# Kernel optimization log

Measured on AMD Instinct MI355X. Metric: run time of the kernel, lower is better.

The kernel has to match this reference:

```python
import jax, jax.numpy as jnp
import numpy as np

N = 1024          # number of junctions
H = 1024          # heatmap height
W = 1024          # heatmap width
NUM_SAMPLES = 64  # samples along each candidate segment (torch_sampler)
DETECT_THRESH = 0.5
INLIER_THRESH = 0.99


def setup_inputs() -> dict:
    key = jax.random.key(0)
    k1, k2 = jax.random.split(key)
    # junctions are (h, w) float coordinates inside the image
    junctions = jax.random.uniform(k1, (N, 2), dtype=jnp.float32) * (H - 1)
    heatmap = jax.random.uniform(k2, (H, W), dtype=jnp.float32)
    return {"junctions": junctions, "heatmap": heatmap}


def _bilinear_sample(heatmap, ch, cw):
    """SOLD2 detect_bilinear: gather 4 corners, bilinear weights. ch/cw: [N,N,S]."""
    hf = jnp.floor(ch); hc = jnp.ceil(ch)
    wf = jnp.floor(cw); wc = jnp.ceil(cw)
    hfi = hf.astype(jnp.int32); hci = hc.astype(jnp.int32)
    wfi = wf.astype(jnp.int32); wci = wc.astype(jnp.int32)
    return (heatmap[hfi, wfi] * (hc - ch) * (wc - cw)
          + heatmap[hfi, wci] * (hc - ch) * (cw - wf)
          + heatmap[hci, wfi] * (ch - hf) * (wc - cw)
          + heatmap[hci, wci] * (ch - hf) * (cw - wf))


def reference(junctions, heatmap):
    n = junctions.shape[0]
    Hh, Ww = heatmap.shape
    t = jnp.linspace(0.0, 1.0, NUM_SAMPLES, dtype=jnp.float32)  # [S]
    # cand_samples[i, j, s] = junc[i] * t[s] + junc[j] * (1 - t[s])  (start=i, end=j)
    ch = junctions[:, None, 0:1] * t + junctions[None, :, 0:1] * (1.0 - t)  # [N,N,S]
    cw = junctions[:, None, 1:2] * t + junctions[None, :, 1:2] * (1.0 - t)  # [N,N,S]
    ch = jnp.clip(ch, 0.0, Hh - 1)
    cw = jnp.clip(cw, 0.0, Ww - 1)
    feat = _bilinear_sample(heatmap, ch, cw)                    # [N,N,S]
    mean_feat = feat.mean(axis=-1)                              # [N,N]
    inlier_ratio = (feat > DETECT_THRESH).astype(jnp.float32).mean(axis=-1)
    # candidate map: strict upper triangle (torch.triu(ones, diagonal=1))
    cand_mask = jnp.triu(jnp.ones((n, n), dtype=bool), k=1)
    detected = (mean_feat > DETECT_THRESH) & (inlier_ratio >= INLIER_THRESH) & cand_mask
    line_map = (detected | detected.T).astype(jnp.int32)        # symmetric line map
    return line_map, mean_feat
```

## Files before the change

kernel.cpp:

```cpp
#include <hip/hip_runtime.h>

#define NJ 1024
#define DETECT 0.5f
#define RESCUE 0.4975f

__device__ __forceinline__ float sample_t(int s) {
    return (s == 63) ? 1.0f : (float)s * (1.0f / 63.0f);
}

__device__ __forceinline__ void exact_pair(const float2 ja, const float2 jb,
                                           const float* __restrict__ heat,
                                           float& mean_o, float& min_o)
{
    float acc = 0.0f;
    float mn  = __builtin_inff();
    for (int s = 0; s < 64; ++s) {
        const float t  = sample_t(s);
        const float om = 1.0f - t;
        float ch = __fadd_rn(__fmul_rn(ja.x, t), __fmul_rn(jb.x, om));
        float cw = __fadd_rn(__fmul_rn(ja.y, t), __fmul_rn(jb.y, om));
        ch = fminf(fmaxf(ch, 0.0f), 1023.0f);
        cw = fminf(fmaxf(cw, 0.0f), 1023.0f);
        const float hf = floorf(ch), hc = ceilf(ch);
        const float wf = floorf(cw), wc = ceilf(cw);
        const int hfi = (int)hf, hci = (int)hc;
        const int wfi = (int)wf, wci = (int)wc;
        const float a00 = heat[(hfi << 10) + wfi];
        const float a01 = heat[(hfi << 10) + wci];
        const float a10 = heat[(hci << 10) + wfi];
        const float a11 = heat[(hci << 10) + wci];
        const float t1 = __fmul_rn(__fmul_rn(a00, __fsub_rn(hc, ch)), __fsub_rn(wc, cw));
        const float t2 = __fmul_rn(__fmul_rn(a01, __fsub_rn(hc, ch)), __fsub_rn(cw, wf));
        const float t3 = __fmul_rn(__fmul_rn(a10, __fsub_rn(ch, hf)), __fsub_rn(wc, cw));
        const float t4 = __fmul_rn(__fmul_rn(a11, __fsub_rn(ch, hf)), __fsub_rn(cw, wf));
        const float feat = __fadd_rn(__fadd_rn(__fadd_rn(t1, t2), t3), t4);
        acc += feat;
        mn = fminf(mn, feat);
    }
    mean_o = acc * (1.0f / 64.0f);
    min_o  = mn;
}

__global__ __launch_bounds__(256) void pack_kernel(
    const float* __restrict__ heat, uint4* __restrict__ packed4)
{
    const int idx = blockIdx.x * 256 + threadIdx.x;
    const int h = idx >> 8;
    const int w4 = (idx & 255) << 2;
    const int hn = (h < 1023) ? h + 1 : 1023;
    const float* r0 = heat + (h  << 10);
    const float* r1 = heat + (hn << 10);
    const float4 a = *(const float4*)(r0 + w4);
    const float4 b = *(const float4*)(r1 + w4);
    const int wnext = (w4 + 4 <= 1023) ? w4 + 4 : 1023;
    const float a4 = r0[wnext];
    const float b4 = r1[wnext];

    const float av[5] = {a.x, a.y, a.z, a.w, a4};
    const float bv[5] = {b.x, b.y, b.z, b.w, b4};
    unsigned int out[4];
    #pragma unroll
    for (int u = 0; u < 4; ++u) {
        const unsigned int c0 = (unsigned int)__float2int_rn(av[u]     * 255.0f);
        const unsigned int c1 = (unsigned int)__float2int_rn(av[u + 1] * 255.0f);
        const unsigned int c2 = (unsigned int)__float2int_rn(bv[u]     * 255.0f);
        const unsigned int c3 = (unsigned int)__float2int_rn(bv[u + 1] * 255.0f);
        out[u] = c0 | (c1 << 8) | (c2 << 16) | (c3 << 24);
    }
    packed4[idx] = make_uint4(out[0], out[1], out[2], out[3]);
}

__global__ __launch_bounds__(256) void sold2_thread_kernel(
    const float* __restrict__ junc,
    const float* __restrict__ heat,
    const unsigned int* __restrict__ packed,
    float* __restrict__ line_out,
    float* __restrict__ mean_out)
{
    const int q = blockIdx.x * 256 + threadIdx.x;
    const int r = q / 513;
    const int c = q - r * 513;
    const int j = (r + c) & 1023;

    const float2 jr  = ((const float2*)junc)[r];
    const float2 jjc = ((const float2*)junc)[j];

    float acc = 0.0f;
    float mn  = __builtin_inff();

    #pragma unroll
    for (int s0 = 0; s0 < 64; s0 += 16) {
        float chv[16], cwv[16];
        unsigned int cv[16];
        #pragma unroll
        for (int u = 0; u < 16; ++u) {
            const int s = s0 + u;
            const float t  = sample_t(s);
            const float om = 1.0f - t;
            float ch = __fadd_rn(__fmul_rn(jr.x, t), __fmul_rn(jjc.x, om));
            float cw = __fadd_rn(__fmul_rn(jr.y, t), __fmul_rn(jjc.y, om));
            ch = fminf(fmaxf(ch, 0.0f), 1023.0f);
            cw = fminf(fmaxf(cw, 0.0f), 1023.0f);
            chv[u] = ch;
            cwv[u] = cw;
            const int hfi = (int)ch;
            const int wfi = (int)cw;
            cv[u] = packed[(hfi << 10) + wfi];
        }
        #pragma unroll
        for (int u = 0; u < 16; ++u) {
            const float ch = chv[u], cw = cwv[u];
            const float hf = floorf(ch), hc = ceilf(ch);
            const float wf = floorf(cw), wc = ceilf(cw);
            const float wh0 = hc - ch, wh1 = ch - hf;
            const float ww0 = wc - cw, ww1 = cw - wf;
            const unsigned int cc = cv[u];
            const float a00 = (float)(cc & 0xffu);
            const float a01 = (float)((cc >> 8) & 0xffu);
            const float a10 = (float)((cc >> 16) & 0xffu);
            const float a11 = (float)(cc >> 24);
            const float feat = a00 * (wh0 * ww0) + a01 * (wh0 * ww1)
                             + a10 * (wh1 * ww0) + a11 * (wh1 * ww1);
            acc += feat;
            mn = fminf(mn, feat);
        }
    }

    float mean = acc * (1.0f / (255.0f * 64.0f));
    const float mns = mn * (1.0f / 255.0f);

    bool det = false;
    if ((mns > RESCUE) && (mean > RESCUE) && (c != 0)) {
        float mn2;
        exact_pair(jr, jjc, heat, mean, mn2);
        det = (mean > DETECT) && (mn2 > DETECT);
    }

    const int p1 = (r << 10) + j;
    __builtin_nontemporal_store(mean, mean_out + p1);
    __builtin_nontemporal_store(det ? 1.0f : 0.0f, line_out + p1);
}

__global__ __launch_bounds__(256) void mirror_kernel(
    float* __restrict__ line_out, float* __restrict__ mean_out)
{
    __shared__ float lm[64][65];
    __shared__ float mm[64][65];
    const int bi = blockIdx.x >> 4;
    const int bj = blockIdx.x & 15;

    const int D = ((bj - bi) << 6) & 1023;
    if (D >= 63 && D <= 449) return;

    const int tx = threadIdx.x & 63;
    const int g  = threadIdx.x >> 6;

    #pragma unroll
    for (int k = 0; k < 16; ++k) {
        const int b = (g << 4) + k;
        const int src = ((bj << 6) + b) * 1024 + (bi << 6) + tx;
        lm[b][tx] = line_out[src];
        mm[b][tx] = mean_out[src];
    }
    __syncthreads();

    #pragma unroll
    for (int k = 0; k < 16; ++k) {
        const int a = (g << 4) + k;
        const int i = (bi << 6) + a;
        const int j = (bj << 6) + tx;
        const int d = (j - i) & 1023;
        if (d >= 513) {
            const int dst = i * 1024 + j;
            __builtin_nontemporal_store(lm[tx][a], line_out + dst);
            __builtin_nontemporal_store(mm[tx][a], mean_out + dst);
        }
    }
}

extern "C" void kernel_launch(void* const* d_in, const int* in_sizes, int n_in,
                              void* d_out, int out_size, void* d_ws, size_t ws_size,
                              hipStream_t stream) {
    const float* junc = (const float*)d_in[0];
    const float* heat = (const float*)d_in[1];
    float* line_out = (float*)d_out;
    float* mean_out = line_out + NJ * NJ;

    unsigned int* packed = (unsigned int*)d_ws;
    pack_kernel<<<1024, 256, 0, stream>>>(heat, (uint4*)packed);

    const int total = NJ * 513;
    sold2_thread_kernel<<<total / 256, 256, 0, stream>>>(junc, heat, packed,
                                                         line_out, mean_out);

    mirror_kernel<<<256, 256, 0, stream>>>(line_out, mean_out);
}
```

Baseline: 186.9 us.

## Software-pipeline packed heatmap gathers with triple-buffered loads and sched barriers

Restructures the sampling loop so three batches of 16 gathers are in flight before any are consumed, rotating buffers so the fourth batch is issued while the first is processed. Sample coordinates are recomputed in the consume phase from opaque copies of the junction values instead of being kept in registers, and scheduling barriers pin the issue/consume order. Launch bounds now request six waves per SIMD to hold occupancy while 48 outstanding loads sit in registers. The aim is to hide gather latency; the cost is extra recomputed arithmetic and higher register pressure, which could cause spills.

```diff
diff --git a/kernel.cpp b/kernel.cpp
--- a/kernel.cpp
+++ b/kernel.cpp
@@ -70,7 +70,7 @@
     packed4[idx] = make_uint4(out[0], out[1], out[2], out[3]);
 }
 
-__global__ __launch_bounds__(256) void sold2_thread_kernel(
+__global__ __launch_bounds__(256, 6) void sold2_thread_kernel(
     const float* __restrict__ junc,
     const float* __restrict__ heat,
     const unsigned int* __restrict__ packed,
@@ -85,46 +85,65 @@
     const float2 jr  = ((const float2*)junc)[r];
     const float2 jjc = ((const float2*)junc)[j];
 
+    float jrx = jr.x, jry = jr.y, jjx = jjc.x, jjy = jjc.y;
+    asm volatile("" : "+v"(jrx), "+v"(jry), "+v"(jjx), "+v"(jjy));
+
     float acc = 0.0f;
     float mn  = __builtin_inff();
 
-    #pragma unroll
-    for (int s0 = 0; s0 < 64; s0 += 16) {
-        float chv[16], cwv[16];
-        unsigned int cv[16];
-        #pragma unroll
-        for (int u = 0; u < 16; ++u) {
-            const int s = s0 + u;
-            const float t  = sample_t(s);
-            const float om = 1.0f - t;
-            float ch = __fadd_rn(__fmul_rn(jr.x, t), __fmul_rn(jjc.x, om));
-            float cw = __fadd_rn(__fmul_rn(jr.y, t), __fmul_rn(jjc.y, om));
-            ch = fminf(fmaxf(ch, 0.0f), 1023.0f);
-            cw = fminf(fmaxf(cw, 0.0f), 1023.0f);
-            chv[u] = ch;
-            cwv[u] = cw;
-            const int hfi = (int)ch;
-            const int wfi = (int)cw;
-            cv[u] = packed[(hfi << 10) + wfi];
-        }
-        #pragma unroll
-        for (int u = 0; u < 16; ++u) {
-            const float ch = chv[u], cw = cwv[u];
-            const float hf = floorf(ch), hc = ceilf(ch);
-            const float wf = floorf(cw), wc = ceilf(cw);
-            const float wh0 = hc - ch, wh1 = ch - hf;
-            const float ww0 = wc - cw, ww1 = cw - wf;
-            const unsigned int cc = cv[u];
-            const float a00 = (float)(cc & 0xffu);
-            const float a01 = (float)((cc >> 8) & 0xffu);
-            const float a10 = (float)((cc >> 16) & 0xffu);
-            const float a11 = (float)(cc >> 24);
-            const float feat = a00 * (wh0 * ww0) + a01 * (wh0 * ww1)
-                             + a10 * (wh1 * ww0) + a11 * (wh1 * ww1);
-            acc += feat;
-            mn = fminf(mn, feat);
-        }
-    }
+    unsigned int cvA[16], cvB[16], cvC[16];
+
+#define ISSUE(S0, CV)                                                         \
+    _Pragma("unroll")                                                         \
+    for (int u = 0; u < 16; ++u) {                                            \
+        const int s = (S0) + u;                                               \
+        const float t  = sample_t(s);                                         \
+        const float om = 1.0f - t;                                            \
+        float ch = __fadd_rn(__fmul_rn(jr.x, t), __fmul_rn(jjc.x, om));       \
+        float cw = __fadd_rn(__fmul_rn(jr.y, t), __fmul_rn(jjc.y, om));       \
+        ch = fminf(fmaxf(ch, 0.0f), 1023.0f);                                 \
+        cw = fminf(fmaxf(cw, 0.0f), 1023.0f);                                 \
+        CV[u] = packed[((int)ch << 10) + (int)cw];                            \
+    }                                                                         \
+    __builtin_amdgcn_sched_barrier(0);
+
+#define CONSUME(S0, CV)                                                       \
+    _Pragma("unroll")                                                         \
+    for (int u = 0; u < 16; ++u) {                                            \
+        const int s = (S0) + u;                                               \
+        const float t  = sample_t(s);                                         \
+        const float om = 1.0f - t;                                            \
+        float ch = __fadd_rn(__fmul_rn(jrx, t), __fmul_rn(jjx, om));          \
+        float cw = __fadd_rn(__fmul_rn(jry, t), __fmul_rn(jjy, om));          \
+        ch = fminf(fmaxf(ch, 0.0f), 1023.0f);                                 \
+        cw = fminf(fmaxf(cw, 0.0f), 1023.0f);                                 \
+        const float hf = floorf(ch), hc = ceilf(ch);                          \
+        const float wf = floorf(cw), wc = ceilf(cw);                          \
+        const float wh0 = hc - ch, wh1 = ch - hf;                             \
+        const float ww0 = wc - cw, ww1 = cw - wf;                             \
+        const unsigned int cc = CV[u];                                        \
+        const float a00 = (float)(cc & 0xffu);                                \
+        const float a01 = (float)((cc >> 8) & 0xffu);                         \
+        const float a10 = (float)((cc >> 16) & 0xffu);                        \
+        const float a11 = (float)(cc >> 24);                                  \
+        const float feat = a00 * (wh0 * ww0) + a01 * (wh0 * ww1)              \
+                         + a10 * (wh1 * ww0) + a11 * (wh1 * ww1);             \
+        acc += feat;                                                          \
+        mn = fminf(mn, feat);                                                 \
+    }                                                                         \
+    __builtin_amdgcn_sched_barrier(0);
+
+    ISSUE(0,  cvA)
+    ISSUE(16, cvB)
+    ISSUE(32, cvC)
+    CONSUME(0,  cvA)
+    ISSUE(48, cvA)
+    CONSUME(16, cvB)
+    CONSUME(32, cvC)
+    CONSUME(48, cvA)
+
+#undef ISSUE
+#undef CONSUME
 
     float mean = acc * (1.0f / (255.0f * 64.0f));
     const float mns = mn * (1.0f / 255.0f);
```

Result: no change. 189.1 us (+1.2%).

## Morton-sort junctions for gather locality and write symmetric outputs directly

Applied to the files above, without the earlier changes.

Adds a single-block bitonic sort that orders the junctions by the Morton code of their integer coordinates. Adjacent threads therefore sample nearby heatmap regions, which should improve cache hit rates for the bilinear gathers. Results are written back through the permutation to both (i,j) and (j,i), so the separate mirror kernel is no longer needed. The cost is scattered, uncoalesced output stores and an extra serial sort launch.

```diff
diff --git a/kernel.cpp b/kernel.cpp
--- a/kernel.cpp
+++ b/kernel.cpp
@@ -70,8 +70,52 @@
     packed4[idx] = make_uint4(out[0], out[1], out[2], out[3]);
 }
 
+__device__ __forceinline__ unsigned int expand_bits16(unsigned int v) {
+    v &= 0x0000FFFFu;
+    v = (v | (v << 8)) & 0x00FF00FFu;
+    v = (v | (v << 4)) & 0x0F0F0F0Fu;
+    v = (v | (v << 2)) & 0x33333333u;
+    v = (v | (v << 1)) & 0x55555555u;
+    return v;
+}
+
+__global__ __launch_bounds__(1024) void sort_kernel(
+    const float* __restrict__ junc, float2* __restrict__ sortedJ,
+    int* __restrict__ perm)
+{
+    __shared__ unsigned int sk[1024];
+    __shared__ unsigned short sv[1024];
+    const int t = threadIdx.x;
+    const float2 jc = ((const float2*)junc)[t];
+    const int mh = min(max((int)jc.x, 0), 1023);
+    const int mw = min(max((int)jc.y, 0), 1023);
+    sk[t] = (expand_bits16((unsigned int)mh) << 1) | expand_bits16((unsigned int)mw);
+    sv[t] = (unsigned short)t;
+    __syncthreads();
+
+    for (unsigned int k = 2; k <= 1024; k <<= 1) {
+        for (unsigned int s = k >> 1; s > 0; s >>= 1) {
+            const int l = t ^ (int)s;
+            if (l > t) {
+                const unsigned int a = sk[t], b = sk[l];
+                const bool up = ((t & k) == 0);
+                if ((a > b) == up) {
+                    sk[t] = b; sk[l] = a;
+                    const unsigned short va = sv[t];
+                    sv[t] = sv[l]; sv[l] = va;
+                }
+            }
+            __syncthreads();
+        }
+    }
+    const int src = (int)sv[t];
+    perm[t] = src;
+    sortedJ[t] = ((const float2*)junc)[src];
+}
+
 __global__ __launch_bounds__(256) void sold2_thread_kernel(
-    const float* __restrict__ junc,
+    const float2* __restrict__ sortedJ,
+    const int* __restrict__ perm,
     const float* __restrict__ heat,
     const unsigned int* __restrict__ packed,
     float* __restrict__ line_out,
@@ -80,10 +124,10 @@
     const int q = blockIdx.x * 256 + threadIdx.x;
     const int r = q / 513;
     const int c = q - r * 513;
-    const int j = (r + c) & 1023;
-
-    const float2 jr  = ((const float2*)junc)[r];
-    const float2 jjc = ((const float2*)junc)[j];
+    const int jc = (r + c) & 1023;
+
+    const float2 jr = sortedJ[r];
+    const float2 jj = sortedJ[jc];
 
     float acc = 0.0f;
     float mn  = __builtin_inff();
@@ -97,8 +141,8 @@
             const int s = s0 + u;
             const float t  = sample_t(s);
             const float om = 1.0f - t;
-            float ch = __fadd_rn(__fmul_rn(jr.x, t), __fmul_rn(jjc.x, om));
-            float cw = __fadd_rn(__fmul_rn(jr.y, t), __fmul_rn(jjc.y, om));
+            float ch = __fadd_rn(__fmul_rn(jr.x, t), __fmul_rn(jj.x, om));
+            float cw = __fadd_rn(__fmul_rn(jr.y, t), __fmul_rn(jj.y, om));
             ch = fminf(fmaxf(ch, 0.0f), 1023.0f);
             cw = fminf(fmaxf(cw, 0.0f), 1023.0f);
             chv[u] = ch;
@@ -132,49 +176,22 @@
     bool det = false;
     if ((mns > RESCUE) && (mean > RESCUE) && (c != 0)) {
         float mn2;
-        exact_pair(jr, jjc, heat, mean, mn2);
+        exact_pair(jr, jj, heat, mean, mn2);
         det = (mean > DETECT) && (mn2 > DETECT);
     }
 
-    const int p1 = (r << 10) + j;
+    const int io = perm[r];
+    const int jo = perm[jc];
+    const float lv = det ? 1.0f : 0.0f;
+
+    const int p1 = (io << 10) + jo;
     __builtin_nontemporal_store(mean, mean_out + p1);
-    __builtin_nontemporal_store(det ? 1.0f : 0.0f, line_out + p1);
-}
-
-__global__ __launch_bounds__(256) void mirror_kernel(
-    float* __restrict__ line_out, float* __restrict__ mean_out)
-{
-    __shared__ float lm[64][65];
-    __shared__ float mm[64][65];
-    const int bi = blockIdx.x >> 4;
-    const int bj = blockIdx.x & 15;
-
-    const int D = ((bj - bi) << 6) & 1023;
-    if (D >= 63 && D <= 449) return;
-
-    const int tx = threadIdx.x & 63;
-    const int g  = threadIdx.x >> 6;
-
-    #pragma unroll
-    for (int k = 0; k < 16; ++k) {
-        const int b = (g << 4) + k;
-        const int src = ((bj << 6) + b) * 1024 + (bi << 6) + tx;
-        lm[b][tx] = line_out[src];
-        mm[b][tx] = mean_out[src];
-    }
-    __syncthreads();
-
-    #pragma unroll
-    for (int k = 0; k < 16; ++k) {
-        const int a = (g << 4) + k;
-        const int i = (bi << 6) + a;
-        const int j = (bj << 6) + tx;
-        const int d = (j - i) & 1023;
-        if (d >= 513) {
-            const int dst = i * 1024 + j;
-            __builtin_nontemporal_store(lm[tx][a], line_out + dst);
-            __builtin_nontemporal_store(mm[tx][a], mean_out + dst);
-        }
+    __builtin_nontemporal_store(lv,   line_out + p1);
+
+    if (c != 0 && c != 512) {
+        const int p2 = (jo << 10) + io;
+        __builtin_nontemporal_store(mean, mean_out + p2);
+        __builtin_nontemporal_store(lv,   line_out + p2);
     }
 }
 
@@ -187,11 +204,13 @@
     float* mean_out = line_out + NJ * NJ;
 
     unsigned int* packed = (unsigned int*)d_ws;
+    float2* sortedJ = (float2*)((char*)d_ws + (4u << 20));
+    int* perm = (int*)((char*)d_ws + (4u << 20) + 8192);
+
     pack_kernel<<<1024, 256, 0, stream>>>(heat, (uint4*)packed);
+    sort_kernel<<<1, 1024, 0, stream>>>(junc, sortedJ, perm);
 
     const int total = NJ * 513;
-    sold2_thread_kernel<<<total / 256, 256, 0, stream>>>(junc, heat, packed,
-                                                         line_out, mean_out);
-
-    mirror_kernel<<<256, 256, 0, stream>>>(line_out, mean_out);
-}
+    sold2_thread_kernel<<<total / 256, 256, 0, stream>>>(sortedJ, perm, heat,
+                                                         packed, line_out, mean_out);
+}
```

New measurement: 181.5 us. -2.9%, faster.
